# Performance work log

Hardware: AMD Instinct MI355X
Metric: run time of the kernel (lower is better)

## Reference

```python
import jax, jax.numpy as jnp
from jax import lax
import numpy as np

L, G, C = 4, 2, 4  # num_blocks, num_sparsity_groups, num_sparsity_cardinals
IMAGE_MEAN = 0.5
SCALE = 2


def _wn(v, g):
    # weight_norm over dims (1,2,3), g per output channel
    n = jnp.sqrt(jnp.sum(v * v, axis=(1, 2, 3), keepdims=True))
    return (g.reshape(-1, 1, 1, 1) / n) * v


def _conv(x, w, b, pad):
    y = lax.conv_general_dilated(x, w, (1, 1), [(pad, pad), (pad, pad)],
                                 dimension_numbers=('NCHW', 'OIHW', 'NCHW'))
    return y + b[None, :, None, None]


def _dyn_conv(x, v, g, b, mw, mb):
    # sparsity-routed conv: per-sample expert mixture of kernels
    w = _wn(v, g)                                   # [G*out, in, k, k]
    B = x.shape[0]
    logits = x.mean((-1, -2)) @ mw.T + mb           # [B, G*C]
    s = jax.nn.softmax(logits.reshape(B, G, C), axis=1)
    wv = w.reshape(G, C, -1, *w.shape[1:])          # [G, C, D, in, k, k]
    wper = jnp.einsum('bgc,gcdikl->bcdikl', s, wv)
    wper = wper.reshape(B, -1, *w.shape[1:])        # [B, out, in, k, k]
    bper = jnp.einsum('bgc,gcd->bcd', s, b.reshape(G, C, -1)).reshape(B, -1)

    def per_sample(xi, wi, bi):
        yi = lax.conv_general_dilated(xi[None], wi, (1, 1), [(1, 1), (1, 1)],
                                      dimension_numbers=('NCHW', 'OIHW', 'NCHW'))[0]
        return yi + bi[:, None, None]

    return jax.vmap(per_sample)(x, wper, bper)


def _pixel_shuffle(x, r):
    B, Cc, H, W = x.shape
    x = x.reshape(B, Cc // (r * r), r, r, H, W)
    x = x.transpose(0, 1, 4, 2, 5, 3)
    return x.reshape(B, Cc // (r * r), H * r, W * r)


def setup_inputs() -> dict:
    key = jax.random.key(0)
    ks = jax.random.split(key, 16)
    f32 = jnp.float32
    inp = {
        'x': jax.random.uniform(ks[0], (8, 3, 64, 64), dtype=f32),
        'head_v': jax.random.normal(ks[1], (64, 3, 3, 3), dtype=f32) * 0.05,
        'head_g': jnp.ones((64,), f32),
        'head_b': jnp.zeros((64,), f32),
        'b1_v': jax.random.normal(ks[2], (L, 512, 64, 3, 3), dtype=f32) * 0.05,
        'b1_g': jnp.full((L, 512), 2.0, f32),
        'b1_b': jnp.zeros((L, 512), f32),
        'b1_mw': jax.random.normal(ks[3], (L, 8, 64), dtype=f32) * 0.05,
        'b1_mb': jax.random.normal(ks[4], (L, 8), dtype=f32) * 0.05,
        'b2_v': jax.random.normal(ks[5], (L, 128, 256, 3, 3), dtype=f32) * 0.05,
        'b2_g': jnp.full((L, 128), 1.0 / np.sqrt(L), f32),
        'b2_b': jnp.zeros((L, 128), f32),
        'b2_mw': jax.random.normal(ks[6], (L, 8, 256), dtype=f32) * 0.05,
        'b2_mb': jax.random.normal(ks[7], (L, 8), dtype=f32) * 0.05,
        'tail_v': jax.random.normal(ks[8], (12, 64, 3, 3), dtype=f32) * 0.05,
        'tail_g': jnp.ones((12,), f32),
        'tail_b': jnp.zeros((12,), f32),
        'skip_v': jax.random.normal(ks[9], (12, 3, 5, 5), dtype=f32) * 0.05,
        'skip_g': jnp.ones((12,), f32),
        'skip_b': jnp.zeros((12,), f32),
    }
    return inp


def reference(x, head_v, head_g, head_b,
              b1_v, b1_g, b1_b, b1_mw, b1_mb,
              b2_v, b2_g, b2_b, b2_mw, b2_mb,
              tail_v, tail_g, tail_b,
              skip_v, skip_g, skip_b):
    x = x - IMAGE_MEAN
    h = _conv(x, _wn(head_v, head_g), head_b, pad=1)
    for l in range(L):
        r0 = h
        t = _dyn_conv(h, b1_v[l], b1_g[l], b1_b[l], b1_mw[l], b1_mb[l])
        t = jax.nn.relu(t)
        t = _dyn_conv(t, b2_v[l], b2_g[l], b2_b[l], b2_mw[l], b2_mb[l])
        h = t + r0
    body = _conv(h, _wn(tail_v, tail_g), tail_b, pad=1)
    s = _conv(x, _wn(skip_v, skip_g), skip_b, pad=2)
    y = _pixel_shuffle(body + s, SCALE) + IMAGE_MEAN
    return y
```

## Files before the change

### kernel.cpp

```cpp
#include <hip/hip_runtime.h>

typedef __attribute__((ext_vector_type(8))) short bf16x8;
typedef __attribute__((ext_vector_type(4))) float f32x4;
typedef __attribute__((ext_vector_type(4))) unsigned short u16x4;
typedef __attribute__((ext_vector_type(8))) unsigned short u16x8;

__device__ __forceinline__ unsigned short bf16u(float x) {
    unsigned int u = __builtin_bit_cast(unsigned int, x);
    unsigned int r = (u + 0x7fffu + ((u >> 16) & 1u)) >> 16;
    return (unsigned short)r;
}
__device__ __forceinline__ void gll16(const void* g, void* l) {
    __builtin_amdgcn_global_load_lds((const __attribute__((address_space(1))) void*)g,
                                     (__attribute__((address_space(3))) void*)l, 16, 0, 0);
}

__global__ __launch_bounds__(256) void zero_all(unsigned short* __restrict__ hbf,
                                                unsigned short* __restrict__ tbf,
                                                float* __restrict__ sums) {
    int i = blockIdx.x * 256 + threadIdx.x;
    u16x8 z8 = {0, 0, 0, 0, 0, 0, 0, 0};
    if (i < 16640) {
        int chv = i & 7, pb = i >> 3, pos = pb % 260, b = pb / 260;
        int y, x;
        if (pos < 66) { y = 0; x = pos; }
        else if (pos < 132) { y = 65; x = pos - 66; }
        else if (pos < 196) { y = pos - 131; x = 0; }
        else { y = pos - 195; x = 65; }
        *(u16x8*)&hbf[(((size_t)b * 66 + y) * 66 + x) * 64 + chv * 8] = z8;
    } else if (i < 83200) {
        int j = i - 16640;
        int chv = j & 7, pb = j >> 3;
        int pos = pb % 260, bc = pb / 260;
        int y, x;
        if (pos < 66) { y = 0; x = pos; }
        else if (pos < 132) { y = 65; x = pos - 66; }
        else if (pos < 196) { y = pos - 131; x = 0; }
        else { y = pos - 195; x = 65; }
        *(u16x8*)&tbf[(((size_t)bc * 66 + y) * 66 + x) * 64 + chv * 8] = z8;
    } else {
        int k = i - 83200;
        f32x4 z4 = {0.f, 0.f, 0.f, 0.f};
        ((f32x4*)sums)[k] = z4;
    }
}

__global__ __launch_bounds__(256) void wn_all(
    const float* __restrict__ hv, const float* __restrict__ hg, float* __restrict__ hw,
    const float* __restrict__ tv, const float* __restrict__ tg, float* __restrict__ tw,
    const float* __restrict__ kv, const float* __restrict__ kg, float* __restrict__ kw,
    const float* __restrict__ b1v, const float* __restrict__ b1g, float* __restrict__ b1s,
    const float* __restrict__ b2v, const float* __restrict__ b2g, float* __restrict__ b2s) {
    int blk = blockIdx.x;
    const float *v, *g;
    float *outw = nullptr, *outs = nullptr;
    int len, row;
    if (blk < 64)        { v = hv;  g = hg;  outw = hw;  len = 27;   row = blk; }
    else if (blk < 76)   { v = tv;  g = tg;  outw = tw;  len = 576;  row = blk - 64; }
    else if (blk < 88)   { v = kv;  g = kg;  outw = kw;  len = 75;   row = blk - 76; }
    else if (blk < 2136) { v = b1v; g = b1g; outs = b1s; len = 576;  row = blk - 88; }
    else                 { v = b2v; g = b2g; outs = b2s; len = 2304; row = blk - 2136; }

    __shared__ float red[4];
    __shared__ float s_sc;
    const float* vr = v + (size_t)row * len;
    float ss = 0.f;
    for (int i = threadIdx.x; i < len; i += 256) { float a = vr[i]; ss += a * a; }
    for (int o = 32; o > 0; o >>= 1) ss += __shfl_down(ss, o);
    if ((threadIdx.x & 63) == 0) red[threadIdx.x >> 6] = ss;
    __syncthreads();
    if (threadIdx.x == 0) s_sc = g[row] / sqrtf(red[0] + red[1] + red[2] + red[3]);
    __syncthreads();
    float sc = s_sc;
    if (outs) {
        if (threadIdx.x == 0) outs[row] = sc;
    } else {
        float* orow = outw + (size_t)row * len;
        for (int i = threadIdx.x; i < len; i += 256) orow[i] = vr[i] * sc;
    }
}

template <int IC, int GOC, int LGG>
__global__ __launch_bounds__(256) void combine_v2(
    const float* __restrict__ v, const float* __restrict__ scale,
    const float* __restrict__ msum, const float* __restrict__ mw,
    const float* __restrict__ mb, float* __restrict__ s_out,
    unsigned short* __restrict__ wq, int D, int OC) {
    constexpr int ROWF = IC * 9;
    constexpr int KCh = IC / 32;
    constexpr int TOTC = GOC * KCh * 9 * 4;
    __shared__ float lv[2 * GOC * ROWF];
    __shared__ float lg[8], sv8[8];
    int tid = threadIdx.x;
    int b = blockIdx.y, ocg = blockIdx.x * GOC;
    {
        int j = tid >> 5, l32 = tid & 31;
        float part = 0.f;
        for (int i = l32; i < IC; i += 32) part += msum[b * IC + i] * mw[j * IC + i];
        for (int m = 16; m > 0; m >>= 1) part += __shfl_xor(part, m);
        if (l32 == 0) lg[j] = part * (1.f / 4096.f) + mb[j];
    }
    for (int i = tid; i < 2 * GOC * ROWF; i += 256) {
        int r = i / ROWF, jj = i - r * ROWF;
        int oc_r = (r / GOC) * OC + ocg + (r % GOC);
        lv[i] = v[(size_t)oc_r * ROWF + jj] * scale[oc_r];
    }
    __syncthreads();
    if (tid < 8) {
        int g = tid >> 2, c = tid & 3;
        float l0 = lg[c], l1 = lg[4 + c];
        float m = fmaxf(l0, l1);
        float e0 = __expf(l0 - m), e1 = __expf(l1 - m);
        float val = ((g == 0) ? e0 : e1) / (e0 + e1);
        sv8[tid] = val;
        if (blockIdx.x == 0) s_out[b * 8 + tid] = val;
    }
    __syncthreads();
    for (int ci = tid; ci < TOTC; ci += 256) {
        int ml = ci & (GOC - 1);
        int c = ci >> LGG;
        int kg = c & 3, c2 = c >> 2;
        int t = c2 % 9, kc = c2 / 9;
        int oc = ocg + ml;
        int cd = oc / D;
        float s0 = sv8[cd], s1 = sv8[4 + cd];
        const float* p0 = &lv[(size_t)ml * ROWF];
        const float* p1 = &lv[(size_t)(GOC + ml) * ROWF];
        u16x8 pk;
#pragma unroll
        for (int kj = 0; kj < 8; ++kj) {
            int ic9 = (kc * 32 + kg * 8 + kj) * 9 + t;
            pk[kj] = bf16u(s0 * p0[ic9] + s1 * p1[ic9]);
        }
        int ot = oc >> 6, mo = oc & 63;
        size_t w_off = ((((size_t)(b * (OC >> 6) + ot) * KCh + kc) * 9 + t) * 4 + kg) * 512 + mo * 8;
        *(u16x8*)&wq[w_off] = pk;
    }
}

__global__ void tail_repack(const float* __restrict__ tw, unsigned short* __restrict__ wq) {
    int idx = blockIdx.x * 256 + threadIdx.x;
    int kj = idx & 7;
    int tmp = idx >> 3;
    int mo = tmp % 16; tmp /= 16;
    int kg = tmp & 3; tmp >>= 2;
    int t = tmp % 9; tmp /= 9;
    int kc = tmp;
    int ic = kc * 32 + kg * 8 + kj;
    float val = (mo < 12) ? tw[((size_t)mo * 64 + ic) * 9 + t] : 0.f;
    wq[idx] = bf16u(val);
}

template <int IC, int OC, int MT, int WM, int WN, int NR,
          bool RELU, bool RES, bool WF32, bool WBF, int OCR, bool DYNB>
__global__ __launch_bounds__(WM * WN * 64, ((WM * WN * 64) == 256) ? 3 : 2)
void conv_mfma(
    const unsigned short* __restrict__ in_bf,
    const unsigned short* __restrict__ wq,
    const float* __restrict__ bias_raw, const float* __restrict__ s8, int lgD,
    const float* __restrict__ res, float* __restrict__ out,
    unsigned short* __restrict__ out_bf, float* __restrict__ msum, long wstride) {
    constexpr int THREADS = WM * WN * 64;
    constexpr int KCH = IC / 32;
    constexpr int NRH = NR + 2;
    constexpr int NT = NR * 64;
    constexpr int NF = (NT / 16) / WN;
    constexpr int MW = MT / (16 * WM);
    constexpr int WELEM = 9 * 32 * MT;
    constexpr int SELEM = NRH * 66 * 32;
    constexpr int SCH = SELEM / 8;
    constexpr int OCB = (OCR % 64 == 0) ? OCR / 64 : 1;

    __shared__ __align__(16) unsigned short S[2][SELEM];
    __shared__ float MRED[WN][MT];

    const int b = blockIdx.z, ot = blockIdx.y;
    const int y0 = blockIdx.x * NR;
    const int tid = threadIdx.x;
    const int lane = tid & 63;
    const int wid = tid >> 6;
    const int wm = wid / WN, wn = wid % WN;
    const int l15 = lane & 15, lk = lane >> 4;
    const int wmo = wm * (MT / WM);
    const int wno = wn * (NT / WN);

    f32x4 acc[MW][NF];
#pragma unroll
    for (int mf = 0; mf < MW; ++mf)
#pragma unroll
        for (int nf = 0; nf < NF; ++nf)
#pragma unroll
            for (int q = 0; q < 4; ++q) acc[mf][nf][q] = 0.f;

    const unsigned short* inb = in_bf + (size_t)b * (IC / 64) * 4356 * 64;
    const unsigned short* wqb = wq + (size_t)b * wstride + (size_t)ot * (KCH * WELEM);
    const unsigned short* wqa = wqb + (size_t)lk * (MT * 8) + (size_t)(wmo + l15) * 8;

    auto STAGE_S = [&](int kc, int buf) {
        const unsigned short* sb = inb + (size_t)(kc >> 1) * (4356 * 64) + (kc & 1) * 32;
        for (int i = tid; i < SCH; i += THREADS) {
            int Lz = i ^ ((i >> 3) & 7);
            int lk2 = Lz & 3, cr = Lz >> 2;
            int col = cr % 66, row = cr / 66;
            gll16(sb + ((size_t)(y0 + row) * 66 + col) * 64 + lk2 * 8,
                  (char*)S[buf] + i * 16);
        }
    };

    STAGE_S(0, 0);
    __syncthreads();
    for (int kc = 0; kc < KCH; ++kc) {
        if (kc + 1 < KCH) STAGE_S(kc + 1, (kc + 1) & 1);
        const unsigned short* Sb = S[kc & 1];
        const unsigned short* wk = wqa + (size_t)kc * 9 * (4 * MT * 8);
        bf16x8 aN[MW];
#pragma unroll
        for (int mf = 0; mf < MW; ++mf)
            aN[mf] = *(const bf16x8*)(wk + mf * 128);
#pragma unroll
        for (int t = 0; t < 9; ++t) {
            const int dy = t / 3, dx = t % 3;
            bf16x8 aC[MW];
#pragma unroll
            for (int mf = 0; mf < MW; ++mf) aC[mf] = aN[mf];
            if (t < 8) {
#pragma unroll
                for (int mf = 0; mf < MW; ++mf)
                    aN[mf] = *(const bf16x8*)(wk + (t + 1) * (4 * MT * 8) + mf * 128);
            }
#pragma unroll
            for (int nf = 0; nf < NF; ++nf) {
                int n = wno + nf * 16 + l15;
                int r = n >> 6, c = n & 63;
                int L = ((r + dy) * 66 + (c + dx)) * 4 + lk;
                int P = L ^ ((L >> 3) & 7);
                bf16x8 bv = *(const bf16x8*)((const char*)Sb + P * 16);
#pragma unroll
                for (int mf = 0; mf < MW; ++mf)
                    acc[mf][nf] = __builtin_amdgcn_mfma_f32_16x16x32_bf16(aC[mf], bv, acc[mf][nf], 0, 0, 0);
            }
        }
        __syncthreads();
    }

    float msr[MW][4];
#pragma unroll
    for (int mf = 0; mf < MW; ++mf) {
        int ocb = ot * MT + wmo + mf * 16 + lk * 4;
        float bv[4];
#pragma unroll
        for (int q = 0; q < 4; ++q) {
            int oc = ocb + q;
            bv[q] = 0.f;
            if (oc < OCR) {
                if (DYNB) {
                    int c = oc >> lgD;
                    bv[q] = s8[b * 8 + c] * bias_raw[oc] + s8[b * 8 + 4 + c] * bias_raw[OCR + oc];
                } else {
                    bv[q] = bias_raw[oc];
                }
            }
            msr[mf][q] = 0.f;
        }
#pragma unroll
        for (int nf = 0; nf < NF; ++nf) {
            int n = wno + nf * 16 + l15;
            int y = y0 + (n >> 6), x = n & 63;
            float vv[4];
#pragma unroll
            for (int q = 0; q < 4; ++q) {
                int oc = ocb + q;
                float v = 0.f;
                if (oc < OCR) {
                    v = acc[mf][nf][q] + bv[q];
                    if (RELU) v = fmaxf(v, 0.f);
                    size_t o = (((size_t)b * OCR + oc) * 64 + y) * 64 + x;
                    if (RES) v += res[o];
                    if (WF32) out[o] = v;
                    msr[mf][q] += v;
                }
                vv[q] = v;
            }
            if (WBF) {
                u16x4 pk;
#pragma unroll
                for (int q = 0; q < 4; ++q) pk[q] = bf16u(vv[q]);
                if (ocb < OCR)
                    *(u16x4*)&out_bf[((((size_t)b * OCB + (ocb >> 6)) * 66 + y + 1) * 66 +
                                      (x + 1)) * 64 + (ocb & 63)] = pk;
            }
        }
    }
    if (msum) {
#pragma unroll
        for (int mf = 0; mf < MW; ++mf)
#pragma unroll
            for (int q = 0; q < 4; ++q) {
                float vq = msr[mf][q];
                vq += __shfl_xor(vq, 1);
                vq += __shfl_xor(vq, 2);
                vq += __shfl_xor(vq, 4);
                vq += __shfl_xor(vq, 8);
                if (l15 == 0) MRED[wn][wmo + mf * 16 + lk * 4 + q] = vq;
            }
        __syncthreads();
        if (tid < MT) {
            float tot = 0.f;
#pragma unroll
            for (int w2 = 0; w2 < WN; ++w2) tot += MRED[w2][tid];
            atomicAdd(&msum[b * OCR + ot * MT + tid], tot);
        }
    }
}

__global__ __launch_bounds__(256) void head_conv(
    const float* __restrict__ in, const float* __restrict__ w,
    const float* __restrict__ bias, float* __restrict__ out,
    unsigned short* __restrict__ out_bf, float* __restrict__ hsum0) {
    constexpr int OCT = 16, IC = 3;
    __shared__ float s_in[34 * 34];
    __shared__ float s_w[OCT * 9];
    __shared__ float wred[4][OCT];
    int b = blockIdx.z;
    int ocBase = blockIdx.y * OCT;
    int ty0 = (blockIdx.x >> 1) * 32;
    int tx0 = (blockIdx.x & 1) * 32;
    int tid = threadIdx.x;
    int lane = tid & 63, wid = tid >> 6;
    int tx = tid & 15, ty = tid >> 4;

    float acc[OCT][4];
#pragma unroll
    for (int oc = 0; oc < OCT; ++oc)
#pragma unroll
        for (int p = 0; p < 4; ++p) acc[oc][p] = 0.f;

    const float* inb = in + (size_t)b * IC * 4096;
    for (int ic = 0; ic < IC; ++ic) {
        const float* src = inb + (size_t)ic * 4096;
        for (int i = tid; i < 34 * 34; i += 256) {
            int r = i / 34, cc = i % 34;
            int gy = ty0 + r - 1, gx = tx0 + cc - 1;
            float val = 0.f;
            if (gy >= 0 && gy < 64 && gx >= 0 && gx < 64) val = src[gy * 64 + gx] - 0.5f;
            s_in[i] = val;
        }
        for (int i = tid; i < OCT * 9; i += 256) {
            int oc = i / 9, t = i % 9;
            s_w[i] = w[((size_t)(ocBase + oc) * IC + ic) * 9 + t];
        }
        __syncthreads();
        float v[4][4];
#pragma unroll
        for (int r = 0; r < 4; ++r)
#pragma unroll
            for (int cc = 0; cc < 4; ++cc) v[r][cc] = s_in[(2 * ty + r) * 34 + (2 * tx + cc)];
#pragma unroll
        for (int oc = 0; oc < OCT; ++oc) {
#pragma unroll
            for (int ky = 0; ky < 3; ++ky)
#pragma unroll
                for (int kx = 0; kx < 3; ++kx) {
                    float wv = s_w[oc * 9 + ky * 3 + kx];
                    acc[oc][0] += wv * v[ky][kx];
                    acc[oc][1] += wv * v[ky][kx + 1];
                    acc[oc][2] += wv * v[ky + 1][kx];
                    acc[oc][3] += wv * v[ky + 1][kx + 1];
                }
        }
        __syncthreads();
    }
    int py = ty0 + 2 * ty, px = tx0 + 2 * tx;
#pragma unroll
    for (int oc = 0; oc < OCT; ++oc) {
        int og = ocBase + oc;
        float bv = bias[og];
        float osum = 0.f;
#pragma unroll
        for (int p = 0; p < 4; ++p) {
            int dy = p >> 1, dx = p & 1;
            float val = acc[oc][p] + bv;
            osum += val;
            out[(((size_t)b * 64 + og) * 64 + py + dy) * 64 + px + dx] = val;
            out_bf[(((size_t)b * 66 + py + dy + 1) * 66 + (px + dx + 1)) * 64 + og] = bf16u(val);
        }
        for (int m = 1; m < 64; m <<= 1) osum += __shfl_xor(osum, m);
        if (lane == 0) wred[wid][oc] = osum;
    }
    __syncthreads();
    if (tid < OCT)
        atomicAdd(&hsum0[b * 64 + ocBase + tid],
                  wred[0][tid] + wred[1][tid] + wred[2][tid] + wred[3][tid]);
}

__global__ __launch_bounds__(256) void shuffle_skip(
    const float* __restrict__ body, const float* __restrict__ x,
    const float* __restrict__ skw, const float* __restrict__ skb,
    float* __restrict__ out) {
    __shared__ float w[900];
    __shared__ float bb[12];
    int tid = threadIdx.x;
    for (int i = tid; i < 900; i += 256) w[i] = skw[i];
    if (tid < 12) bb[tid] = skb[tid];
    __syncthreads();
    int idx = blockIdx.x * 256 + tid;
    int ox = idx & 127;
    int oy = (idx >> 7) & 127;
    int v = idx >> 14;
    int c = v % 3;
    int b = v / 3;
    int rx = ox & 1, ry = oy & 1;
    int xx = ox >> 1, yy = oy >> 1;
    int ch = c * 4 + ry * 2 + rx;
    float acc = bb[ch];
    for (int ic = 0; ic < 3; ++ic)
        for (int ky = 0; ky < 5; ++ky) {
            int gy = yy + ky - 2;
            if (gy < 0 || gy >= 64) continue;
            for (int kx = 0; kx < 5; ++kx) {
                int gx = xx + kx - 2;
                if (gx < 0 || gx >= 64) continue;
                acc += w[((ch * 3 + ic) * 5 + ky) * 5 + kx] *
                       (x[((size_t)(b * 3 + ic) * 64 + gy) * 64 + gx] - 0.5f);
            }
        }
    size_t src = (((size_t)b * 12 + ch) * 64 + yy) * 64 + xx;
    out[idx] = body[src] + acc + 0.5f;
}

extern "C" void kernel_launch(void* const* d_in, const int* in_sizes, int n_in,
                              void* d_out, int out_size, void* d_ws, size_t ws_size,
                              hipStream_t stream) {
    const float* x      = (const float*)d_in[0];
    const float* head_v = (const float*)d_in[1];
    const float* head_g = (const float*)d_in[2];
    const float* head_b = (const float*)d_in[3];
    const float* b1_v   = (const float*)d_in[4];
    const float* b1_g   = (const float*)d_in[5];
    const float* b1_b   = (const float*)d_in[6];
    const float* b1_mw  = (const float*)d_in[7];
    const float* b1_mb  = (const float*)d_in[8];
    const float* b2_v   = (const float*)d_in[9];
    const float* b2_g   = (const float*)d_in[10];
    const float* b2_b   = (const float*)d_in[11];
    const float* b2_mw  = (const float*)d_in[12];
    const float* b2_mb  = (const float*)d_in[13];
    const float* tail_v = (const float*)d_in[14];
    const float* tail_g = (const float*)d_in[15];
    const float* tail_b = (const float*)d_in[16];
    const float* skip_v = (const float*)d_in[17];
    const float* skip_g = (const float*)d_in[18];
    const float* skip_b = (const float*)d_in[19];

    float* ws = (float*)d_ws;
    size_t off = 0;
    auto alloc = [&](size_t n) { float* p = ws + off; off += (n + 3) & ~(size_t)3; return p; };
    float* head_w = alloc(64 * 27);
    float* tail_w = alloc(12 * 576);
    float* skip_w = alloc(12 * 75);
    float* b1_sc  = alloc(2048);
    float* b2_sc  = alloc(512);
    float* h      = alloc((size_t)8 * 64 * 4096);
    float* sums   = alloc(10240);
    float* sbuf   = alloc(64);
    float* body   = alloc((size_t)8 * 12 * 4096);
    unsigned short* wq1  = (unsigned short*)alloc((size_t)8 * 256 * 576 / 2);
    unsigned short* wq2  = (unsigned short*)alloc((size_t)8 * 64 * 2304 / 2);
    unsigned short* wqt  = (unsigned short*)alloc(9216 / 2);
    unsigned short* h_bf = (unsigned short*)alloc((size_t)8 * 66 * 66 * 64 / 2);
    unsigned short* t_bf = (unsigned short*)alloc((size_t)8 * 4 * 66 * 66 * 64 / 2);
    (void)ws_size; (void)in_sizes; (void)n_in; (void)out_size;

    auto hsum = [&](int l) { return sums + l * 512; };
    auto tsum = [&](int l) { return sums + 2048 + l * 2048; };

    zero_all<<<335, 256, 0, stream>>>(h_bf, t_bf, sums);
    wn_all<<<2648, 256, 0, stream>>>(head_v, head_g, head_w, tail_v, tail_g, tail_w,
                                     skip_v, skip_g, skip_w, b1_v, b1_g, b1_sc,
                                     b2_v, b2_g, b2_sc);
    head_conv<<<dim3(4, 4, 8), 256, 0, stream>>>(x, head_w, head_b, h, h_bf, hsum(0));
    tail_repack<<<36, 256, 0, stream>>>(tail_w, wqt);

    for (int l = 0; l < 4; ++l) {
        combine_v2<64, 4, 2><<<dim3(64, 8), 256, 0, stream>>>(
            b1_v + (size_t)l * 512 * 576, b1_sc + (size_t)l * 512, hsum(l),
            b1_mw + (size_t)l * 8 * 64, b1_mb + l * 8, sbuf, wq1, 64, 256);
        conv_mfma<64, 256, 64, 1, 4, 4, true, false, false, true, 256, true>
            <<<dim3(16, 4, 8), 256, 0, stream>>>(h_bf, wq1, b1_b + (size_t)l * 512, sbuf, 6,
                                                 nullptr, nullptr, t_bf, tsum(l), 147456);
        combine_v2<256, 2, 1><<<dim3(32, 8), 256, 0, stream>>>(
            b2_v + (size_t)l * 128 * 2304, b2_sc + (size_t)l * 128, tsum(l),
            b2_mw + (size_t)l * 8 * 256, b2_mb + l * 8, sbuf, wq2, 16, 64);
        conv_mfma<256, 64, 64, 2, 4, 2, false, true, true, true, 64, true>
            <<<dim3(32, 1, 8), 512, 0, stream>>>(t_bf, wq2, b2_b + (size_t)l * 128, sbuf, 4,
                                                 h, h, h_bf, (l < 3) ? hsum(l + 1) : nullptr,
                                                 147456);
    }

    conv_mfma<64, 16, 16, 1, 4, 4, false, false, true, false, 12, false>
        <<<dim3(16, 1, 8), 256, 0, stream>>>(h_bf, wqt, tail_b, nullptr, 0,
                                             nullptr, body, nullptr, nullptr, 0);
    shuffle_skip<<<1536, 256, 0, stream>>>(body, x, skip_w, skip_b, (float*)d_out);
}
```

Before: 356.4 us.

## Switch activations to 32-channel bf16 chunks and drop the fp32 residual stream

```diff
diff --git a/kernel.cpp b/kernel.cpp
--- a/kernel.cpp
+++ b/kernel.cpp
@@ -2,13 +2,15 @@
 
 typedef __attribute__((ext_vector_type(8))) short bf16x8;
 typedef __attribute__((ext_vector_type(4))) float f32x4;
-typedef __attribute__((ext_vector_type(4))) unsigned short u16x4;
 typedef __attribute__((ext_vector_type(8))) unsigned short u16x8;
 
 __device__ __forceinline__ unsigned short bf16u(float x) {
     unsigned int u = __builtin_bit_cast(unsigned int, x);
     unsigned int r = (u + 0x7fffu + ((u >> 16) & 1u)) >> 16;
     return (unsigned short)r;
+}
+__device__ __forceinline__ float bf2f(unsigned short u) {
+    return __builtin_bit_cast(float, (unsigned int)u << 16);
 }
 __device__ __forceinline__ void gll16(const void* g, void* l) {
     __builtin_amdgcn_global_load_lds((const __attribute__((address_space(1))) void*)g,
@@ -21,23 +23,22 @@
     int i = blockIdx.x * 256 + threadIdx.x;
     u16x8 z8 = {0, 0, 0, 0, 0, 0, 0, 0};
     if (i < 16640) {
-        int chv = i & 7, pb = i >> 3, pos = pb % 260, b = pb / 260;
+        int chv = i & 3, pb = i >> 2, pos = pb % 260, bc = pb / 260;
         int y, x;
         if (pos < 66) { y = 0; x = pos; }
         else if (pos < 132) { y = 65; x = pos - 66; }
         else if (pos < 196) { y = pos - 131; x = 0; }
         else { y = pos - 195; x = 65; }
-        *(u16x8*)&hbf[(((size_t)b * 66 + y) * 66 + x) * 64 + chv * 8] = z8;
+        *(u16x8*)&hbf[((size_t)bc * 4356 + y * 66 + x) * 32 + chv * 8] = z8;
     } else if (i < 83200) {
         int j = i - 16640;
-        int chv = j & 7, pb = j >> 3;
-        int pos = pb % 260, bc = pb / 260;
+        int chv = j & 3, pb = j >> 2, pos = pb % 260, bc = pb / 260;
         int y, x;
         if (pos < 66) { y = 0; x = pos; }
         else if (pos < 132) { y = 65; x = pos - 66; }
         else if (pos < 196) { y = pos - 131; x = 0; }
         else { y = pos - 195; x = 65; }
-        *(u16x8*)&tbf[(((size_t)bc * 66 + y) * 66 + x) * 64 + chv * 8] = z8;
+        *(u16x8*)&tbf[((size_t)bc * 4356 + y * 66 + x) * 32 + chv * 8] = z8;
     } else {
         int k = i - 83200;
         f32x4 z4 = {0.f, 0.f, 0.f, 0.f};
@@ -80,7 +81,7 @@
     }
 }
 
-template <int IC, int GOC, int LGG>
+template <int IC, int GOC, int LGG, int LGMO>
 __global__ __launch_bounds__(256) void combine_v2(
     const float* __restrict__ v, const float* __restrict__ scale,
     const float* __restrict__ msum, const float* __restrict__ mw,
@@ -132,8 +133,8 @@
             int ic9 = (kc * 32 + kg * 8 + kj) * 9 + t;
             pk[kj] = bf16u(s0 * p0[ic9] + s1 * p1[ic9]);
         }
-        int ot = oc >> 6, mo = oc & 63;
-        size_t w_off = ((((size_t)(b * (OC >> 6) + ot) * KCh + kc) * 9 + t) * 4 + kg) * 512 + mo * 8;
+        size_t w_off = ((((size_t)(b * (OC >> LGMO) + (oc >> LGMO)) * KCh + kc) * 9 + t) * 4 + kg)
+                           * ((1 << LGMO) * 8) + (size_t)(oc & ((1 << LGMO) - 1)) * 8;
         *(u16x8*)&wq[w_off] = pk;
     }
 }
@@ -152,13 +153,13 @@
 }
 
 template <int IC, int OC, int MT, int WM, int WN, int NR,
-          bool RELU, bool RES, bool WF32, bool WBF, int OCR, bool DYNB>
-__global__ __launch_bounds__(WM * WN * 64, ((WM * WN * 64) == 256) ? 3 : 2)
+          bool RELU, bool RES, bool WF32, bool WBF, int OCR, bool DYNB, int MINW>
+__global__ __launch_bounds__(WM * WN * 64, MINW)
 void conv_mfma(
     const unsigned short* __restrict__ in_bf,
     const unsigned short* __restrict__ wq,
     const float* __restrict__ bias_raw, const float* __restrict__ s8, int lgD,
-    const float* __restrict__ res, float* __restrict__ out,
+    float* __restrict__ out,
     unsigned short* __restrict__ out_bf, float* __restrict__ msum, long wstride) {
     constexpr int THREADS = WM * WN * 64;
     constexpr int KCH = IC / 32;
@@ -169,12 +170,12 @@
     constexpr int WELEM = 9 * 32 * MT;
     constexpr int SELEM = NRH * 66 * 32;
     constexpr int SCH = SELEM / 8;
-    constexpr int OCB = (OCR % 64 == 0) ? OCR / 64 : 1;
+    constexpr int OCB = OCR / 32;
 
     __shared__ __align__(16) unsigned short S[2][SELEM];
     __shared__ float MRED[WN][MT];
 
-    const int b = blockIdx.z, ot = blockIdx.y;
+    const int b = blockIdx.y, ot = blockIdx.z;
     const int y0 = blockIdx.x * NR;
     const int tid = threadIdx.x;
     const int lane = tid & 63;
@@ -192,17 +193,17 @@
 #pragma unroll
             for (int q = 0; q < 4; ++q) acc[mf][nf][q] = 0.f;
 
-    const unsigned short* inb = in_bf + (size_t)b * (IC / 64) * 4356 * 64;
+    const unsigned short* inb = in_bf + (size_t)b * KCH * (4356 * 32);
     const unsigned short* wqb = wq + (size_t)b * wstride + (size_t)ot * (KCH * WELEM);
     const unsigned short* wqa = wqb + (size_t)lk * (MT * 8) + (size_t)(wmo + l15) * 8;
 
     auto STAGE_S = [&](int kc, int buf) {
-        const unsigned short* sb = inb + (size_t)(kc >> 1) * (4356 * 64) + (kc & 1) * 32;
+        const unsigned short* sb = inb + (size_t)kc * (4356 * 32);
         for (int i = tid; i < SCH; i += THREADS) {
             int Lz = i ^ ((i >> 3) & 7);
             int lk2 = Lz & 3, cr = Lz >> 2;
             int col = cr % 66, row = cr / 66;
-            gll16(sb + ((size_t)(y0 + row) * 66 + col) * 64 + lk2 * 8,
+            gll16(sb + ((size_t)(y0 + row) * 66 + col) * 32 + lk2 * 8,
                   (char*)S[buf] + i * 16);
         }
     };
@@ -212,11 +213,11 @@
     for (int kc = 0; kc < KCH; ++kc) {
         if (kc + 1 < KCH) STAGE_S(kc + 1, (kc + 1) & 1);
         const unsigned short* Sb = S[kc & 1];
-        const unsigned short* wk = wqa + (size_t)kc * 9 * (4 * MT * 8);
+        const unsigned short* wk = wqa + (size_t)kc * WELEM;
         bf16x8 aN[MW];
 #pragma unroll
         for (int mf = 0; mf < MW; ++mf)
-            aN[mf] = *(const bf16x8*)(wk + mf * 128);
+            aN[mf] = *(const bf16x8*)(wk + mf * (16 * 8));
 #pragma unroll
         for (int t = 0; t < 9; ++t) {
             const int dy = t / 3, dx = t % 3;
@@ -226,7 +227,7 @@
             if (t < 8) {
 #pragma unroll
                 for (int mf = 0; mf < MW; ++mf)
-                    aN[mf] = *(const bf16x8*)(wk + (t + 1) * (4 * MT * 8) + mf * 128);
+                    aN[mf] = *(const bf16x8*)(wk + (t + 1) * (4 * MT * 8) + mf * (16 * 8));
             }
 #pragma unroll
             for (int nf = 0; nf < NF; ++nf) {
@@ -243,79 +244,111 @@
         __syncthreads();
     }
 
-    float msr[MW][4];
-#pragma unroll
-    for (int mf = 0; mf < MW; ++mf) {
-        int ocb = ot * MT + wmo + mf * 16 + lk * 4;
-        float bv[4];
-#pragma unroll
-        for (int q = 0; q < 4; ++q) {
-            int oc = ocb + q;
-            bv[q] = 0.f;
-            if (oc < OCR) {
-                if (DYNB) {
-                    int c = oc >> lgD;
-                    bv[q] = s8[b * 8 + c] * bias_raw[oc] + s8[b * 8 + 4 + c] * bias_raw[OCR + oc];
-                } else {
-                    bv[q] = bias_raw[oc];
-                }
-            }
-            msr[mf][q] = 0.f;
-        }
-#pragma unroll
-        for (int nf = 0; nf < NF; ++nf) {
-            int n = wno + nf * 16 + l15;
-            int y = y0 + (n >> 6), x = n & 63;
-            float vv[4];
+    if constexpr (WBF) {
+        static_assert(NF == 2, "shuffle epilogue needs NF==2");
+        const int mynf = lk & 1;
+        const int ch = lk >> 1;
+        const bool evenlk = ((lk & 1) == 0);
+#pragma unroll
+        for (int mf = 0; mf < MW; ++mf) {
+            int ocb = ot * MT + wmo + mf * 16 + lk * 4;
+            float bvv[4];
 #pragma unroll
             for (int q = 0; q < 4; ++q) {
                 int oc = ocb + q;
-                float v = 0.f;
-                if (oc < OCR) {
-                    v = acc[mf][nf][q] + bv[q];
+                if (DYNB) {
+                    int cc = oc >> lgD;
+                    bvv[q] = s8[b * 8 + cc] * bias_raw[oc] + s8[b * 8 + 4 + cc] * bias_raw[OCR + oc];
+                } else {
+                    bvv[q] = bias_raw[oc];
+                }
+            }
+            float r[2][4], pr[2][4];
+#pragma unroll
+            for (int nf = 0; nf < 2; ++nf)
+#pragma unroll
+                for (int q = 0; q < 4; ++q) {
+                    float v = acc[mf][nf][q] + bvv[q];
                     if (RELU) v = fmaxf(v, 0.f);
-                    size_t o = (((size_t)b * OCR + oc) * 64 + y) * 64 + x;
-                    if (RES) v += res[o];
-                    if (WF32) out[o] = v;
-                    msr[mf][q] += v;
+                    r[nf][q] = v;
                 }
-                vv[q] = v;
-            }
-            if (WBF) {
-                u16x4 pk;
-#pragma unroll
-                for (int q = 0; q < 4; ++q) pk[q] = bf16u(vv[q]);
-                if (ocb < OCR)
-                    *(u16x4*)&out_bf[((((size_t)b * OCB + (ocb >> 6)) * 66 + y + 1) * 66 +
-                                      (x + 1)) * 64 + (ocb & 63)] = pk;
-            }
-        }
-    }
-    if (msum) {
-#pragma unroll
-        for (int mf = 0; mf < MW; ++mf)
+#pragma unroll
+            for (int nf = 0; nf < 2; ++nf)
+#pragma unroll
+                for (int q = 0; q < 4; ++q) pr[nf][q] = __shfl_xor(r[nf][q], 16);
+            float v8[8];
 #pragma unroll
             for (int q = 0; q < 4; ++q) {
-                float vq = msr[mf][q];
-                vq += __shfl_xor(vq, 1);
-                vq += __shfl_xor(vq, 2);
-                vq += __shfl_xor(vq, 4);
-                vq += __shfl_xor(vq, 8);
-                if (l15 == 0) MRED[wn][wmo + mf * 16 + lk * 4 + q] = vq;
-            }
-        __syncthreads();
-        if (tid < MT) {
-            float tot = 0.f;
-#pragma unroll
-            for (int w2 = 0; w2 < WN; ++w2) tot += MRED[w2][tid];
-            atomicAdd(&msum[b * OCR + ot * MT + tid], tot);
+                float a = r[mynf][q], p = pr[mynf][q];
+                v8[q] = evenlk ? a : p;
+                v8[4 + q] = evenlk ? p : a;
+            }
+            int n = wno + mynf * 16 + l15;
+            int y = y0 + (n >> 6), x = n & 63;
+            int occ = ot * MT + wmo + mf * 16 + ch * 8;
+            size_t addr = ((((size_t)b * OCB + (occ >> 5)) * 66 + (y + 1)) * 66 + (x + 1)) * 32
+                          + (occ & 31);
+            if (RES) {
+                u16x8 rv = *(const u16x8*)&out_bf[addr];
+#pragma unroll
+                for (int j = 0; j < 8; ++j) v8[j] += bf2f(rv[j]);
+            }
+            u16x8 pk;
+#pragma unroll
+            for (int j = 0; j < 8; ++j) pk[j] = bf16u(v8[j]);
+            *(u16x8*)&out_bf[addr] = pk;
+            if (msum) {
+#pragma unroll
+                for (int j = 0; j < 8; ++j) {
+                    float t = v8[j];
+                    t += __shfl_xor(t, 1);
+                    t += __shfl_xor(t, 2);
+                    t += __shfl_xor(t, 4);
+                    t += __shfl_xor(t, 8);
+                    t += __shfl_xor(t, 16);
+                    v8[j] = t;
+                }
+                if ((lane & 31) == 0) {
+#pragma unroll
+                    for (int j = 0; j < 8; ++j)
+                        MRED[wn][wmo + mf * 16 + ch * 8 + j] = v8[j];
+                }
+            }
+        }
+        if (msum) {
+            __syncthreads();
+            if (tid < MT) {
+                float tot = 0.f;
+#pragma unroll
+                for (int w2 = 0; w2 < WN; ++w2) tot += MRED[w2][tid];
+                atomicAdd(&msum[b * OCR + ot * MT + tid], tot);
+            }
+        }
+    }
+    if constexpr (WF32) {
+#pragma unroll
+        for (int mf = 0; mf < MW; ++mf) {
+            int ocb = ot * MT + wmo + mf * 16 + lk * 4;
+#pragma unroll
+            for (int nf = 0; nf < NF; ++nf) {
+                int n = wno + nf * 16 + l15;
+                int y = y0 + (n >> 6), x = n & 63;
+#pragma unroll
+                for (int q = 0; q < 4; ++q) {
+                    int oc = ocb + q;
+                    if (oc < OCR) {
+                        float v = acc[mf][nf][q] + bias_raw[oc];
+                        out[(((size_t)b * OCR + oc) * 64 + y) * 64 + x] = v;
+                    }
+                }
+            }
         }
     }
 }
 
 __global__ __launch_bounds__(256) void head_conv(
     const float* __restrict__ in, const float* __restrict__ w,
-    const float* __restrict__ bias, float* __restrict__ out,
+    const float* __restrict__ bias,
     unsigned short* __restrict__ out_bf, float* __restrict__ hsum0) {
     constexpr int OCT = 16, IC = 3;
     __shared__ float s_in[34 * 34];
@@ -381,8 +414,8 @@
             int dy = p >> 1, dx = p & 1;
             float val = acc[oc][p] + bv;
             osum += val;
-            out[(((size_t)b * 64 + og) * 64 + py + dy) * 64 + px + dx] = val;
-            out_bf[(((size_t)b * 66 + py + dy + 1) * 66 + (px + dx + 1)) * 64 + og] = bf16u(val);
+            out_bf[((size_t)(b * 2 + (og >> 5)) * 4356 + (py + dy + 1) * 66 + (px + dx + 1)) * 32
+                   + (og & 31)] = bf16u(val);
         }
         for (int m = 1; m < 64; m <<= 1) osum += __shfl_xor(osum, m);
         if (lane == 0) wred[wid][oc] = osum;
@@ -460,15 +493,14 @@
     float* skip_w = alloc(12 * 75);
     float* b1_sc  = alloc(2048);
     float* b2_sc  = alloc(512);
-    float* h      = alloc((size_t)8 * 64 * 4096);
     float* sums   = alloc(10240);
     float* sbuf   = alloc(64);
     float* body   = alloc((size_t)8 * 12 * 4096);
     unsigned short* wq1  = (unsigned short*)alloc((size_t)8 * 256 * 576 / 2);
     unsigned short* wq2  = (unsigned short*)alloc((size_t)8 * 64 * 2304 / 2);
     unsigned short* wqt  = (unsigned short*)alloc(9216 / 2);
-    unsigned short* h_bf = (unsigned short*)alloc((size_t)8 * 66 * 66 * 64 / 2);
-    unsigned short* t_bf = (unsigned short*)alloc((size_t)8 * 4 * 66 * 66 * 64 / 2);
+    unsigned short* h_bf = (unsigned short*)alloc((size_t)8 * 2 * 4356 * 32 / 2);
+    unsigned short* t_bf = (unsigned short*)alloc((size_t)8 * 8 * 4356 * 32 / 2);
     (void)ws_size; (void)in_sizes; (void)n_in; (void)out_size;
 
     auto hsum = [&](int l) { return sums + l * 512; };
@@ -478,27 +510,27 @@
     wn_all<<<2648, 256, 0, stream>>>(head_v, head_g, head_w, tail_v, tail_g, tail_w,
                                      skip_v, skip_g, skip_w, b1_v, b1_g, b1_sc,
                                      b2_v, b2_g, b2_sc);
-    head_conv<<<dim3(4, 4, 8), 256, 0, stream>>>(x, head_w, head_b, h, h_bf, hsum(0));
+    head_conv<<<dim3(4, 4, 8), 256, 0, stream>>>(x, head_w, head_b, h_bf, hsum(0));
     tail_repack<<<36, 256, 0, stream>>>(tail_w, wqt);
 
     for (int l = 0; l < 4; ++l) {
-        combine_v2<64, 4, 2><<<dim3(64, 8), 256, 0, stream>>>(
+        combine_v2<64, 4, 2, 5><<<dim3(64, 8), 256, 0, stream>>>(
             b1_v + (size_t)l * 512 * 576, b1_sc + (size_t)l * 512, hsum(l),
             b1_mw + (size_t)l * 8 * 64, b1_mb + l * 8, sbuf, wq1, 64, 256);
-        conv_mfma<64, 256, 64, 1, 4, 4, true, false, false, true, 256, true>
-            <<<dim3(16, 4, 8), 256, 0, stream>>>(h_bf, wq1, b1_b + (size_t)l * 512, sbuf, 6,
-                                                 nullptr, nullptr, t_bf, tsum(l), 147456);
-        combine_v2<256, 2, 1><<<dim3(32, 8), 256, 0, stream>>>(
+        conv_mfma<64, 256, 32, 1, 4, 2, true, false, false, true, 256, true, 4>
+            <<<dim3(32, 8, 8), 256, 0, stream>>>(h_bf, wq1, b1_b + (size_t)l * 512, sbuf, 6,
+                                                 nullptr, t_bf, tsum(l), 147456);
+        combine_v2<256, 2, 1, 6><<<dim3(32, 8), 256, 0, stream>>>(
             b2_v + (size_t)l * 128 * 2304, b2_sc + (size_t)l * 128, tsum(l),
             b2_mw + (size_t)l * 8 * 256, b2_mb + l * 8, sbuf, wq2, 16, 64);
-        conv_mfma<256, 64, 64, 2, 4, 2, false, true, true, true, 64, true>
-            <<<dim3(32, 1, 8), 512, 0, stream>>>(t_bf, wq2, b2_b + (size_t)l * 128, sbuf, 4,
-                                                 h, h, h_bf, (l < 3) ? hsum(l + 1) : nullptr,
+        conv_mfma<256, 64, 64, 2, 4, 2, false, true, false, true, 64, true, 2>
+            <<<dim3(32, 8, 1), 512, 0, stream>>>(t_bf, wq2, b2_b + (size_t)l * 128, sbuf, 4,
+                                                 nullptr, h_bf, (l < 3) ? hsum(l + 1) : nullptr,
                                                  147456);
     }
 
-    conv_mfma<64, 16, 16, 1, 4, 4, false, false, true, false, 12, false>
-        <<<dim3(16, 1, 8), 256, 0, stream>>>(h_bf, wqt, tail_b, nullptr, 0,
-                                             nullptr, body, nullptr, nullptr, 0);
+    conv_mfma<64, 16, 16, 1, 4, 4, false, false, true, false, 12, false, 2>
+        <<<dim3(16, 8, 1), 256, 0, stream>>>(h_bf, wqt, tail_b, nullptr, 0,
+                                             body, nullptr, nullptr, 0);
     shuffle_skip<<<1536, 256, 0, stream>>>(body, x, skip_w, skip_b, (float*)d_out);
 }
```

Measured after the change: 336.8 us. 5.5% less time.
